# Optimization experiments

Measured on AMD Instinct MI355X. Metric: run time of the kernel, lower is better.

Reference implementation:

```python
import jax, jax.numpy as jnp
import numpy as np

N_FQK, N_FV, N_REL, N_VAL, N_KNOW = 512, 256, 128, 64, 256
TOPK_QK, TOPK_V, TOPK_REL, TOPK_VAL = 64, 32, 16, 3
FQK_END = N_FQK
FV_END = N_FQK + N_FV
REL_END = FV_END + N_REL
VAL_END = REL_END + N_VAL
TOTAL = VAL_END + N_KNOW


def setup_inputs() -> dict:
    key = jax.random.key(0)
    k1, k2, k3, k4, k5 = jax.random.split(key, 5)
    B, S, D, DS = 8, 4096, 1024, 64
    x = jax.random.normal(k1, (B, S, D), dtype=jnp.float32)
    importance = jax.random.uniform(k2, (B, S), dtype=jnp.float32)
    proj_w = jax.random.normal(k3, (DS, D), dtype=jnp.float32) * (1.0 / np.sqrt(D))
    proj_b = jax.random.normal(k4, (DS,), dtype=jnp.float32) * 0.01
    neuron_emb = jax.random.normal(k5, (TOTAL, DS), dtype=jnp.float32) * 0.02
    return {"x": x, "importance": importance, "proj_w": proj_w,
            "proj_b": proj_b, "neuron_emb": neuron_emb}


def _topk_sparsify(w, k):
    # keep top-k values per row, zero elsewhere
    vals, idx = jax.lax.top_k(w, k)
    B = w.shape[0]
    sparse = jnp.zeros_like(w).at[jnp.arange(B)[:, None], idx].set(vals)
    return sparse, idx


def reference(x, importance, proj_w, proj_b, neuron_emb):
    # shared projection + normalized neuron embeddings (eval: dropout off,
    # no excitability bonus)
    h = jnp.einsum('bsd,kd->bsk', x, proj_w) + proj_b          # [B,S,d_space]
    emb_n = neuron_emb / jnp.linalg.norm(neuron_emb, axis=-1, keepdims=True)
    all_logits = jnp.einsum('bsk,nk->bsn', h, emb_n)            # [B,S,TOTAL]

    def agg(logits):
        pref = jax.nn.softmax(logits, axis=-1)                  # [B,S,n]
        return jnp.einsum('bs,bsn->bn', importance, pref)

    w_qk = agg(all_logits[..., :FQK_END])
    _, idx_qk = jax.lax.top_k(w_qk, TOPK_QK)
    idx_qk = jnp.sort(idx_qk, axis=-1)

    w_v = agg(all_logits[..., FQK_END:FV_END])
    _, idx_v = jax.lax.top_k(w_v, TOPK_V)
    idx_v = jnp.sort(idx_v, axis=-1)

    rel_logits = all_logits[..., FV_END:REL_END]
    # relational_Q and relational_K use the same logits slice (eval mode)
    rel_dense_Q = agg(rel_logits)
    rel_dense_K = agg(rel_logits)
    rel_Q, _ = _topk_sparsify(rel_dense_Q, TOPK_REL)
    rel_K, _ = _topk_sparsify(rel_dense_K, TOPK_REL)

    val_dense = agg(all_logits[..., REL_END:VAL_END])
    val_w, _ = _topk_sparsify(val_dense, TOPK_VAL)

    return idx_qk, idx_v, rel_Q, rel_K, val_w
```

## Files before the change

kernel.cpp:

```cpp
#include <hip/hip_runtime.h>


typedef short short8 __attribute__((ext_vector_type(8)));
typedef float f32x4 __attribute__((ext_vector_type(4)));
typedef unsigned int uint4v __attribute__((ext_vector_type(4)));

__device__ __forceinline__ unsigned short f32_to_bf16(float f) {
  unsigned u = __float_as_uint(f);
  u += 0x7FFF + ((u >> 16) & 1);
  return (unsigned short)(u >> 16);
}
__device__ __forceinline__ float bf16_to_f32(unsigned short h) {
  return __uint_as_float(((unsigned)h) << 16);
}

__device__ __forceinline__ unsigned cvt_pk_bf16(float a, float b) {
  unsigned r;
  asm("v_cvt_pk_bf16_f32 %0, %1, %2" : "=v"(r) : "v"(a), "v"(b));
  return r;
}

__device__ __forceinline__ void split8v(const f32x4& v0, const f32x4& v1,
                                        short8& hi, short8& lo) {
  unsigned hp[4], lp[4];
#pragma unroll
  for (int j = 0; j < 4; ++j) {
    float a = (j < 2) ? v0[2 * j] : v1[2 * j - 4];
    float b = (j < 2) ? v0[2 * j + 1] : v1[2 * j - 3];
    unsigned p = cvt_pk_bf16(a, b);
    float ra = a - __uint_as_float(p << 16);
    float rb = b - __uint_as_float(p & 0xFFFF0000u);
    hp[j] = p;
    lp[j] = cvt_pk_bf16(ra, rb);
  }
  hi = __builtin_bit_cast(short8, (uint4v){hp[0], hp[1], hp[2], hp[3]});
  lo = __builtin_bit_cast(short8, (uint4v){lp[0], lp[1], lp[2], lp[3]});
}

#define MFMA(a, b, c) __builtin_amdgcn_mfma_f32_16x16x32_bf16(a, b, c, 0, 0, 0)
#define WAITVM(n) asm volatile("s_waitcnt vmcnt(" #n ")" ::: "memory")

typedef const __attribute__((address_space(1))) unsigned int guint;
typedef __attribute__((address_space(3))) unsigned int luint;
__device__ __forceinline__ void stage16(const float* g, float* l) {
  __builtin_amdgcn_global_load_lds((guint*)g, (luint*)l, 16, 0, 0);
}
__device__ __forceinline__ void bar() {
  asm volatile("" ::: "memory");
  __builtin_amdgcn_s_barrier();
  asm volatile("" ::: "memory");
}

__global__ __launch_bounds__(256) void k_prep(const float* __restrict__ pw,
                                              const float* __restrict__ emb,
                                              unsigned short* __restrict__ whi,
                                              unsigned short* __restrict__ wlo,
                                              unsigned short* __restrict__ ehi,
                                              unsigned short* __restrict__ elo) {
  int tid = blockIdx.x * 256 + threadIdx.x;
  for (int i = tid; i < 65536; i += gridDim.x * 256) {
    float v = pw[i];
    unsigned short h = f32_to_bf16(v);
    whi[i] = h;
    wlo[i] = f32_to_bf16(v - bf16_to_f32(h));
  }
  int wid = tid >> 6, lane = tid & 63;
  int nw = gridDim.x * 4;
  for (int n = wid; n < 960; n += nw) {
    float v = emb[n * 64 + lane];
    float s = v * v;
#pragma unroll
    for (int off = 1; off < 64; off <<= 1) s += __shfl_xor(s, off);
    float vn = v / sqrtf(s);
    unsigned short h = f32_to_bf16(vn);
    ehi[n * 64 + lane] = h;
    elo[n * 64 + lane] = f32_to_bf16(vn - bf16_to_f32(h));
  }
}

__global__ __launch_bounds__(256, 4) void k_main(
    const float* __restrict__ x, const unsigned short* __restrict__ whi,
    const unsigned short* __restrict__ wlo, const float* __restrict__ pb,
    const unsigned short* __restrict__ ehi, const unsigned short* __restrict__ elo,
    const float* __restrict__ imp, float* __restrict__ pp) {
  __shared__ __align__(16) float xt[5][32][32];
  __shared__ __align__(16) unsigned short hxh[32][64];
  __shared__ __align__(16) unsigned short hxl[32][64];
  __shared__ float zpart[4][32][4];
  __shared__ float coefL[32][4];

  const int tid = threadIdx.x, w = tid >> 6, lane = tid & 63;
  const int q = lane >> 4, c = lane & 15;
  const int row0 = blockIdx.x * 32;
  const int nt0 = w;
  const int koff = blockIdx.x & 31;

  const int srow = tid >> 3;
  const int scol = ((tid & 7) ^ (srow & 7)) * 4;
  const float* sbase = x + (size_t)(row0 + srow) * 1024 + scol;
  auto STAGEX = [&](int slot, int ks) {
    int kp = (ks + koff) & 31;
    stage16(sbase + kp * 32, &xt[slot][0][0] + (w << 8));
  };

  const unsigned short* bwh = whi + (size_t)(nt0 * 16 + c) * 1024 + q * 8;
  const unsigned short* bwl = wlo + (size_t)(nt0 * 16 + c) * 1024 + q * 8;

  f32x4 acc0 = {0.f, 0.f, 0.f, 0.f}, acc1 = {0.f, 0.f, 0.f, 0.f};

  const unsigned sw = (unsigned)((c & 7) << 4);
  const unsigned off1 = ((unsigned)(q * 32)) ^ sw;
  const unsigned off2 = ((unsigned)(q * 32 + 16)) ^ sw;
  const char* xby = (const char*)&xt[0][0][0] + (size_t)c * 128;

  int rs = 0, wsl = 4;
  auto projstep = [&](short8 B_hi, short8 B_lo) {
    const char* bp = xby + rs * 4096;
    f32x4 a0 = *(const f32x4*)(bp + off1);
    f32x4 a1 = *(const f32x4*)(bp + off2);
    f32x4 a2 = *(const f32x4*)(bp + 2048 + off1);
    f32x4 a3 = *(const f32x4*)(bp + 2048 + off2);
    short8 ah, al;
    split8v(a0, a1, ah, al);
    acc0 = MFMA(ah, B_hi, acc0);
    acc0 = MFMA(ah, B_lo, acc0);
    acc0 = MFMA(al, B_hi, acc0);
    split8v(a2, a3, ah, al);
    acc1 = MFMA(ah, B_hi, acc1);
    acc1 = MFMA(ah, B_lo, acc1);
    acc1 = MFMA(al, B_hi, acc1);
    ++rs; if (rs == 5) rs = 0;
  };
  auto loadB = [&](short8 (&h)[2], short8 (&l)[2], int g) {
    int k0 = (2 * g + koff) & 31, k1 = (2 * g + 1 + koff) & 31;
    h[0] = *(const short8*)(bwh + k0 * 32);
    h[1] = *(const short8*)(bwh + k1 * 32);
    l[0] = *(const short8*)(bwl + k0 * 32);
    l[1] = *(const short8*)(bwl + k1 * 32);
  };

  short8 BhA[2], BlA[2], BhB[2], BlB[2];
  loadB(BhA, BlA, 0);
  STAGEX(0, 0); STAGEX(1, 1); STAGEX(2, 2); STAGEX(3, 3);

  auto gpair = [&](int g) {
    loadB(BhB, BlB, g + 1);
    WAITVM(6); bar();
    STAGEX(wsl, 2 * g + 4); ++wsl; if (wsl == 5) wsl = 0;
    projstep(BhA[0], BlA[0]);
    WAITVM(7); bar();
    STAGEX(wsl, 2 * g + 5); ++wsl; if (wsl == 5) wsl = 0;
    projstep(BhA[1], BlA[1]);
    loadB(BhA, BlA, g + 2);
    WAITVM(6); bar();
    STAGEX(wsl, 2 * g + 6); ++wsl; if (wsl == 5) wsl = 0;
    projstep(BhB[0], BlB[0]);
    WAITVM(7); bar();
    STAGEX(wsl, 2 * g + 7); ++wsl; if (wsl == 5) wsl = 0;
    projstep(BhB[1], BlB[1]);
  };
  gpair(0); gpair(2); gpair(4); gpair(6); gpair(8); gpair(10); gpair(12);
  loadB(BhB, BlB, 15);
  WAITVM(7); bar(); projstep(BhA[0], BlA[0]);
  WAITVM(6); bar(); projstep(BhA[1], BlA[1]);
  WAITVM(1); bar(); projstep(BhB[0], BlB[0]);
  WAITVM(0); bar(); projstep(BhB[1], BlB[1]);

  float bias = pb[nt0 * 16 + c];
#pragma unroll
  for (int mt = 0; mt < 2; ++mt) {
    f32x4 a = mt ? acc1 : acc0;
#pragma unroll
    for (int r = 0; r < 4; ++r) {
      float val = a[r] + bias;
      int row = mt * 16 + q * 4 + r;
      unsigned colb = (unsigned)((nt0 * 16 + c) * 2);
      unsigned o = (unsigned)(row * 128) + (colb ^ ((unsigned)(row & 7) << 4));
      unsigned short h = f32_to_bf16(val);
      *(unsigned short*)((char*)&hxh[0][0] + o) = h;
      *(unsigned short*)((char*)&hxl[0][0] + o) = f32_to_bf16(val - bf16_to_f32(h));
    }
  }
  __syncthreads();

  short8 Ahi[2][2], Alo[2][2];
#pragma unroll
  for (int mt = 0; mt < 2; ++mt) {
    int row = mt * 16 + c;
    unsigned rsw = (unsigned)((row & 7) << 4);
#pragma unroll
    for (int k2 = 0; k2 < 2; ++k2) {
      unsigned o = (unsigned)(row * 128) + (((unsigned)(k2 * 64 + q * 16)) ^ rsw);
      Ahi[mt][k2] = *(const short8*)((const char*)&hxh[0][0] + o);
      Alo[mt][k2] = *(const short8*)((const char*)&hxl[0][0] + o);
    }
  }

  const size_t ebq = (size_t)c * 64 + q * 8;
  short8 eA[4], eB[4];
  auto LOADE = [&](short8 (&d)[4], int i) {
    size_t eb = (size_t)(w + 4 * i) * 1024 + ebq;
    d[0] = *(const short8*)(ehi + eb);
    d[1] = *(const short8*)(ehi + eb + 32);
    d[2] = *(const short8*)(elo + eb);
    d[3] = *(const short8*)(elo + eb + 32);
  };
  auto logits = [&](int mt, short8 (&e)[4]) -> f32x4 {
    f32x4 la = {0.f, 0.f, 0.f, 0.f}, lb = {0.f, 0.f, 0.f, 0.f};
    la = MFMA(Ahi[mt][0], e[0], la); la = MFMA(Ahi[mt][1], e[1], la);
    lb = MFMA(Ahi[mt][0], e[2], lb); lb = MFMA(Ahi[mt][1], e[3], lb);
    lb = MFMA(Alo[mt][0], e[0], lb); lb = MFMA(Alo[mt][1], e[1], lb);
    return la + lb;
  };

  f32x4 zacc0 = {0.f, 0.f, 0.f, 0.f}, zacc1 = {0.f, 0.f, 0.f, 0.f};
  auto zflush = [&](int seg) {
#pragma unroll
    for (int mt = 0; mt < 2; ++mt)
#pragma unroll
      for (int r = 0; r < 4; ++r) {
        float v = mt ? zacc1[r] : zacc0[r];
        v += __shfl_xor(v, 1); v += __shfl_xor(v, 2);
        v += __shfl_xor(v, 4); v += __shfl_xor(v, 8);
        if (c == 0) zpart[w][mt * 16 + q * 4 + r][seg] = v;
      }
    zacc0 = (f32x4){0.f, 0.f, 0.f, 0.f};
    zacc1 = (f32x4){0.f, 0.f, 0.f, 0.f};
  };

  int cur_seg = 0;
  auto step1 = [&](int i, short8 (&e)[4]) {
    int nt = w + 4 * i;
    int s = (nt < 32) ? 0 : (nt < 48) ? 1 : (nt < 56) ? 2 : 3;
    if (s != cur_seg) { zflush(cur_seg); cur_seg = s; }
    f32x4 l0 = logits(0, e), l1 = logits(1, e);
#pragma unroll
    for (int r = 0; r < 4; ++r) {
      zacc0[r] += __expf(l0[r]);
      zacc1[r] += __expf(l1[r]);
    }
  };
  LOADE(eA, 0);
#pragma unroll 1
  for (int j = 0; j < 7; ++j) {
    LOADE(eB, 2 * j + 1); step1(2 * j, eA);
    LOADE(eA, 2 * j + 2); step1(2 * j + 1, eB);
  }
  step1(14, eA);
  zflush(cur_seg);
  __syncthreads();
  if (tid < 128) {
    int row = tid & 31, sg = tid >> 5;
    float Z = zpart[0][row][sg] + zpart[1][row][sg] + zpart[2][row][sg] + zpart[3][row][sg];
    coefL[row][sg] = imp[row0 + row] / Z;
  }
  __syncthreads();

  float* ppb = pp + (size_t)blockIdx.x * 960;
  f32x4 cf0, cf1;
  int cs2 = -1;
  auto step2 = [&](int i, short8 (&e)[4]) {
    int nt = w + 4 * i;
    int s = (nt < 32) ? 0 : (nt < 48) ? 1 : (nt < 56) ? 2 : 3;
    if (s != cs2) {
#pragma unroll
      for (int r = 0; r < 4; ++r) {
        cf0[r] = coefL[q * 4 + r][s];
        cf1[r] = coefL[16 + q * 4 + r][s];
      }
      cs2 = s;
    }
    f32x4 l0 = logits(0, e), l1 = logits(1, e);
    float wsum = 0.f;
#pragma unroll
    for (int r = 0; r < 4; ++r) {
      wsum = fmaf(__expf(l0[r]), cf0[r], wsum);
      wsum = fmaf(__expf(l1[r]), cf1[r], wsum);
    }
    wsum += __shfl_xor(wsum, 16);
    wsum += __shfl_xor(wsum, 32);
    if (lane < 16) ppb[nt * 16 + c] = wsum;
  };
  LOADE(eA, 0);
#pragma unroll 1
  for (int j = 0; j < 7; ++j) {
    LOADE(eB, 2 * j + 1); step2(2 * j, eA);
    LOADE(eA, 2 * j + 2); step2(2 * j + 1, eB);
  }
  step2(14, eA);
}

__global__ __launch_bounds__(256) void k_topk(const float* __restrict__ pp,
                                              float* __restrict__ out) {
  __shared__ float vals[512];
  __shared__ int flags[512];
  int blk = blockIdx.x;
  int b = blk >> 2, t = blk & 3;
  int tid = threadIdx.x;
  const int Ns[4] = {512, 256, 128, 64};
  const int Ks[4] = {64, 32, 16, 3};
  const int Off[4] = {0, 512, 768, 896};
  int N = Ns[t], K = Ks[t], off = Off[t];
  for (int n = tid; n < N; n += 256) {
    const float* p = pp + (size_t)(b * 128) * 960 + off + n;
    float s0 = 0.f, s1 = 0.f, s2 = 0.f, s3 = 0.f;
    for (int rb = 0; rb < 128; rb += 4) {
      s0 += p[(size_t)(rb + 0) * 960];
      s1 += p[(size_t)(rb + 1) * 960];
      s2 += p[(size_t)(rb + 2) * 960];
      s3 += p[(size_t)(rb + 3) * 960];
    }
    vals[n] = (s0 + s1) + (s2 + s3);
  }
  __syncthreads();
  for (int n = tid; n < N; n += 256) {
    float v = vals[n];
    int rank = 0;
    for (int m = 0; m < N; ++m) {
      float u = vals[m];
      rank += (u > v || (u == v && m < n)) ? 1 : 0;
    }
    flags[n] = (rank < K) ? 1 : 0;
  }
  __syncthreads();
  if (t <= 1) {
    if (tid < 64) {
      int base = 0;
      for (int ch = 0; ch < N; ch += 64) {
        int n = ch + tid;
        int f = flags[n];
        unsigned long long mask = __ballot(f);
        if (f) {
          int pos = base + __popcll(mask & ((1ull << tid) - 1ull));
          if (t == 0) out[b * 64 + pos] = (float)n;
          else out[512 + b * 32 + pos] = (float)n;
        }
        base += __popcll(mask);
      }
    }
  } else if (t == 2) {
    for (int n = tid; n < 128; n += 256) {
      float v = flags[n] ? vals[n] : 0.f;
      out[768 + b * 128 + n] = v;
      out[1792 + b * 128 + n] = v;
    }
  } else {
    for (int n = tid; n < 64; n += 256) {
      float v = flags[n] ? vals[n] : 0.f;
      out[2816 + b * 64 + n] = v;
    }
  }
}

extern "C" void kernel_launch(void* const* d_in, const int* in_sizes, int n_in,
                              void* d_out, int out_size, void* d_ws, size_t ws_size,
                              hipStream_t stream) {
  const float* x   = (const float*)d_in[0];
  const float* imp = (const float*)d_in[1];
  const float* pw  = (const float*)d_in[2];
  const float* pb  = (const float*)d_in[3];
  const float* emb = (const float*)d_in[4];
  float* out = (float*)d_out;

  char* ws = (char*)d_ws;
  unsigned short* whi = (unsigned short*)(ws);
  unsigned short* wlo = (unsigned short*)(ws + 131072);
  unsigned short* ehi = (unsigned short*)(ws + 262144);
  unsigned short* elo = (unsigned short*)(ws + 385024);
  float*          pp  = (float*)(ws + 507904);

  hipLaunchKernelGGL(k_prep, dim3(64), dim3(256), 0, stream, pw, emb, whi, wlo, ehi, elo);
  hipLaunchKernelGGL(k_main, dim3(1024), dim3(256), 0, stream, x, whi, wlo, pb, ehi, elo, imp, pp);
  hipLaunchKernelGGL(k_topk, dim3(32), dim3(256), 0, stream, pp, out);
}
```

Before: 326.4 us.

## Halve row tile per block, interleave hi/lo weights, split partial reduction kernel

The main kernel now processes 16 rows per block instead of 32, so twice as many blocks run, with occupancy raised to 8 blocks per CU and a 3-slot, 64-wide x staging ring. Weights and embeddings are stored with hi/lo bf16 halves interleaved so each lane reads them from nearby addresses. The per-batch column reduction of partial sums moves into a separate, wider-parallel kernel ahead of top-k. The aim is more latency hiding and a cheaper tail, at the cost of fewer MFMAs per B-fragment load (half the reuse of weights per block), twice as many partial rows, and an extra kernel launch.

```diff
diff --git a/kernel.cpp b/kernel.cpp
--- a/kernel.cpp
+++ b/kernel.cpp
@@ -53,16 +53,17 @@
 
 __global__ __launch_bounds__(256) void k_prep(const float* __restrict__ pw,
                                               const float* __restrict__ emb,
-                                              unsigned short* __restrict__ whi,
-                                              unsigned short* __restrict__ wlo,
-                                              unsigned short* __restrict__ ehi,
-                                              unsigned short* __restrict__ elo) {
+                                              unsigned short* __restrict__ W2,
+                                              unsigned short* __restrict__ E2) {
   int tid = blockIdx.x * 256 + threadIdx.x;
   for (int i = tid; i < 65536; i += gridDim.x * 256) {
     float v = pw[i];
     unsigned short h = f32_to_bf16(v);
-    whi[i] = h;
-    wlo[i] = f32_to_bf16(v - bf16_to_f32(h));
+    int col = i >> 10, d = i & 1023;
+    int ks = d >> 5, q = (d >> 3) & 3, j = d & 7;
+    int idx = col * 2048 + ks * 64 + q * 16 + j;
+    W2[idx] = h;
+    W2[idx + 8] = f32_to_bf16(v - bf16_to_f32(h));
   }
   int wid = tid >> 6, lane = tid & 63;
   int nw = gridDim.x * 4;
@@ -73,159 +74,143 @@
     for (int off = 1; off < 64; off <<= 1) s += __shfl_xor(s, off);
     float vn = v / sqrtf(s);
     unsigned short h = f32_to_bf16(vn);
-    ehi[n * 64 + lane] = h;
-    elo[n * 64 + lane] = f32_to_bf16(vn - bf16_to_f32(h));
-  }
-}
-
-__global__ __launch_bounds__(256, 4) void k_main(
-    const float* __restrict__ x, const unsigned short* __restrict__ whi,
-    const unsigned short* __restrict__ wlo, const float* __restrict__ pb,
-    const unsigned short* __restrict__ ehi, const unsigned short* __restrict__ elo,
+    int idx = n * 128 + (lane >> 3) * 16 + (lane & 7);
+    E2[idx] = h;
+    E2[idx + 8] = f32_to_bf16(vn - bf16_to_f32(h));
+  }
+}
+
+__global__ __launch_bounds__(256, 8) void k_main(
+    const float* __restrict__ x, const unsigned short* __restrict__ W2,
+    const float* __restrict__ pb, const unsigned short* __restrict__ E2,
     const float* __restrict__ imp, float* __restrict__ pp) {
-  __shared__ __align__(16) float xt[5][32][32];
-  __shared__ __align__(16) unsigned short hxh[32][64];
-  __shared__ __align__(16) unsigned short hxl[32][64];
-  __shared__ float zpart[4][32][4];
-  __shared__ float coefL[32][4];
+  __shared__ __align__(16) float xt[3][16][64];
+  __shared__ __align__(16) unsigned short hxh[16][64];
+  __shared__ __align__(16) unsigned short hxl[16][64];
+  __shared__ float zpart[4][16][4];
+  __shared__ float coefL[16][4];
 
   const int tid = threadIdx.x, w = tid >> 6, lane = tid & 63;
   const int q = lane >> 4, c = lane & 15;
-  const int row0 = blockIdx.x * 32;
+  const int row0 = blockIdx.x * 16;
   const int nt0 = w;
-  const int koff = blockIdx.x & 31;
-
-  const int srow = tid >> 3;
-  const int scol = ((tid & 7) ^ (srow & 7)) * 4;
-  const float* sbase = x + (size_t)(row0 + srow) * 1024 + scol;
-  auto STAGEX = [&](int slot, int ks) {
-    int kp = (ks + koff) & 31;
-    stage16(sbase + kp * 32, &xt[slot][0][0] + (w << 8));
-  };
-
-  const unsigned short* bwh = whi + (size_t)(nt0 * 16 + c) * 1024 + q * 8;
-  const unsigned short* bwl = wlo + (size_t)(nt0 * 16 + c) * 1024 + q * 8;
-
-  f32x4 acc0 = {0.f, 0.f, 0.f, 0.f}, acc1 = {0.f, 0.f, 0.f, 0.f};
-
-  const unsigned sw = (unsigned)((c & 7) << 4);
-  const unsigned off1 = ((unsigned)(q * 32)) ^ sw;
-  const unsigned off2 = ((unsigned)(q * 32 + 16)) ^ sw;
-  const char* xby = (const char*)&xt[0][0][0] + (size_t)c * 128;
-
-  int rs = 0, wsl = 4;
-  auto projstep = [&](short8 B_hi, short8 B_lo) {
-    const char* bp = xby + rs * 4096;
-    f32x4 a0 = *(const f32x4*)(bp + off1);
-    f32x4 a1 = *(const f32x4*)(bp + off2);
-    f32x4 a2 = *(const f32x4*)(bp + 2048 + off1);
-    f32x4 a3 = *(const f32x4*)(bp + 2048 + off2);
+  const int uoff = blockIdx.x & 15;
+
+  const int srow = tid >> 4;
+  const int p16 = tid & 15;
+  const int lslot = (p16 & 8) | ((p16 & 7) ^ (srow & 7));
+  const float* sbase = x + (size_t)(row0 + srow) * 1024 + lslot * 4;
+  auto STAGEX = [&](int slot, int u) {
+    int up = (u + uoff) & 15;
+    stage16(sbase + up * 64, &xt[slot][0][0] + (w << 8));
+  };
+
+  const unsigned short* bw = W2 + (size_t)(nt0 * 16 + c) * 2048 + q * 16;
+
+  f32x4 acc = {0.f, 0.f, 0.f, 0.f};
+
+  const unsigned o0a = (unsigned)(c * 256 + (((q * 2) ^ (c & 7)) << 4));
+  const unsigned o0b = (unsigned)(c * 256 + (((q * 2 + 1) ^ (c & 7)) << 4));
+  const char* xbase = (const char*)&xt[0][0][0];
+
+  int rs = 0, wsl = 2;
+  auto projstep2 = [&](short8 (&bh)[2], short8 (&bl)[2]) {
+    const char* bp = xbase + rs * 4096;
+    f32x4 a0 = *(const f32x4*)(bp + o0a);
+    f32x4 a1 = *(const f32x4*)(bp + o0b);
     short8 ah, al;
     split8v(a0, a1, ah, al);
-    acc0 = MFMA(ah, B_hi, acc0);
-    acc0 = MFMA(ah, B_lo, acc0);
-    acc0 = MFMA(al, B_hi, acc0);
-    split8v(a2, a3, ah, al);
-    acc1 = MFMA(ah, B_hi, acc1);
-    acc1 = MFMA(ah, B_lo, acc1);
-    acc1 = MFMA(al, B_hi, acc1);
-    ++rs; if (rs == 5) rs = 0;
-  };
-  auto loadB = [&](short8 (&h)[2], short8 (&l)[2], int g) {
-    int k0 = (2 * g + koff) & 31, k1 = (2 * g + 1 + koff) & 31;
-    h[0] = *(const short8*)(bwh + k0 * 32);
-    h[1] = *(const short8*)(bwh + k1 * 32);
-    l[0] = *(const short8*)(bwl + k0 * 32);
-    l[1] = *(const short8*)(bwl + k1 * 32);
+    acc = MFMA(ah, bh[0], acc);
+    acc = MFMA(ah, bl[0], acc);
+    acc = MFMA(al, bh[0], acc);
+    a0 = *(const f32x4*)(bp + o0a + 128);
+    a1 = *(const f32x4*)(bp + o0b + 128);
+    split8v(a0, a1, ah, al);
+    acc = MFMA(ah, bh[1], acc);
+    acc = MFMA(ah, bl[1], acc);
+    acc = MFMA(al, bh[1], acc);
+    ++rs; if (rs == 3) rs = 0;
+  };
+  auto loadB = [&](short8 (&h)[2], short8 (&l)[2], int u) {
+    int ku = (u + uoff) & 15;
+    const unsigned short* f = bw + ku * 128;
+    h[0] = *(const short8*)(f);
+    l[0] = *(const short8*)(f + 8);
+    h[1] = *(const short8*)(f + 64);
+    l[1] = *(const short8*)(f + 72);
   };
 
   short8 BhA[2], BlA[2], BhB[2], BlB[2];
   loadB(BhA, BlA, 0);
-  STAGEX(0, 0); STAGEX(1, 1); STAGEX(2, 2); STAGEX(3, 3);
-
-  auto gpair = [&](int g) {
-    loadB(BhB, BlB, g + 1);
-    WAITVM(6); bar();
-    STAGEX(wsl, 2 * g + 4); ++wsl; if (wsl == 5) wsl = 0;
-    projstep(BhA[0], BlA[0]);
-    WAITVM(7); bar();
-    STAGEX(wsl, 2 * g + 5); ++wsl; if (wsl == 5) wsl = 0;
-    projstep(BhA[1], BlA[1]);
-    loadB(BhA, BlA, g + 2);
-    WAITVM(6); bar();
-    STAGEX(wsl, 2 * g + 6); ++wsl; if (wsl == 5) wsl = 0;
-    projstep(BhB[0], BlB[0]);
-    WAITVM(7); bar();
-    STAGEX(wsl, 2 * g + 7); ++wsl; if (wsl == 5) wsl = 0;
-    projstep(BhB[1], BlB[1]);
-  };
-  gpair(0); gpair(2); gpair(4); gpair(6); gpair(8); gpair(10); gpair(12);
+  STAGEX(0, 0); STAGEX(1, 1);
+  auto unit = [&](int u, short8 (&ch)[2], short8 (&cl)[2],
+                  short8 (&nh)[2], short8 (&nl)[2]) {
+    loadB(nh, nl, u + 1);
+    WAITVM(5); bar();
+    STAGEX(wsl, u + 2); ++wsl; if (wsl == 3) wsl = 0;
+    projstep2(ch, cl);
+  };
+  unit(0, BhA, BlA, BhB, BlB);  unit(1, BhB, BlB, BhA, BlA);
+  unit(2, BhA, BlA, BhB, BlB);  unit(3, BhB, BlB, BhA, BlA);
+  unit(4, BhA, BlA, BhB, BlB);  unit(5, BhB, BlB, BhA, BlA);
+  unit(6, BhA, BlA, BhB, BlB);  unit(7, BhB, BlB, BhA, BlA);
+  unit(8, BhA, BlA, BhB, BlB);  unit(9, BhB, BlB, BhA, BlA);
+  unit(10, BhA, BlA, BhB, BlB); unit(11, BhB, BlB, BhA, BlA);
+  unit(12, BhA, BlA, BhB, BlB); unit(13, BhB, BlB, BhA, BlA);
   loadB(BhB, BlB, 15);
-  WAITVM(7); bar(); projstep(BhA[0], BlA[0]);
-  WAITVM(6); bar(); projstep(BhA[1], BlA[1]);
-  WAITVM(1); bar(); projstep(BhB[0], BlB[0]);
-  WAITVM(0); bar(); projstep(BhB[1], BlB[1]);
+  WAITVM(5); bar(); projstep2(BhA, BlA);
+  WAITVM(0); bar(); projstep2(BhB, BlB);
 
   float bias = pb[nt0 * 16 + c];
 #pragma unroll
-  for (int mt = 0; mt < 2; ++mt) {
-    f32x4 a = mt ? acc1 : acc0;
-#pragma unroll
-    for (int r = 0; r < 4; ++r) {
-      float val = a[r] + bias;
-      int row = mt * 16 + q * 4 + r;
-      unsigned colb = (unsigned)((nt0 * 16 + c) * 2);
-      unsigned o = (unsigned)(row * 128) + (colb ^ ((unsigned)(row & 7) << 4));
-      unsigned short h = f32_to_bf16(val);
-      *(unsigned short*)((char*)&hxh[0][0] + o) = h;
-      *(unsigned short*)((char*)&hxl[0][0] + o) = f32_to_bf16(val - bf16_to_f32(h));
-    }
-  }
-  __syncthreads();
-
-  short8 Ahi[2][2], Alo[2][2];
-#pragma unroll
-  for (int mt = 0; mt < 2; ++mt) {
-    int row = mt * 16 + c;
-    unsigned rsw = (unsigned)((row & 7) << 4);
+  for (int r = 0; r < 4; ++r) {
+    float val = acc[r] + bias;
+    int row = q * 4 + r;
+    unsigned colb = (unsigned)((nt0 * 16 + c) * 2);
+    unsigned o = (unsigned)(row * 128) + (colb ^ ((unsigned)(row & 7) << 4));
+    unsigned short h = f32_to_bf16(val);
+    *(unsigned short*)((char*)&hxh[0][0] + o) = h;
+    *(unsigned short*)((char*)&hxl[0][0] + o) = f32_to_bf16(val - bf16_to_f32(h));
+  }
+  __syncthreads();
+
+  short8 Ahi[2], Alo[2];
+  {
+    unsigned rsw = (unsigned)((c & 7) << 4);
 #pragma unroll
     for (int k2 = 0; k2 < 2; ++k2) {
-      unsigned o = (unsigned)(row * 128) + (((unsigned)(k2 * 64 + q * 16)) ^ rsw);
-      Ahi[mt][k2] = *(const short8*)((const char*)&hxh[0][0] + o);
-      Alo[mt][k2] = *(const short8*)((const char*)&hxl[0][0] + o);
-    }
-  }
-
-  const size_t ebq = (size_t)c * 64 + q * 8;
+      unsigned o = (unsigned)(c * 128) + (((unsigned)(k2 * 64 + q * 16)) ^ rsw);
+      Ahi[k2] = *(const short8*)((const char*)&hxh[0][0] + o);
+      Alo[k2] = *(const short8*)((const char*)&hxl[0][0] + o);
+    }
+  }
+
   short8 eA[4], eB[4];
   auto LOADE = [&](short8 (&d)[4], int i) {
-    size_t eb = (size_t)(w + 4 * i) * 1024 + ebq;
-    d[0] = *(const short8*)(ehi + eb);
-    d[1] = *(const short8*)(ehi + eb + 32);
-    d[2] = *(const short8*)(elo + eb);
-    d[3] = *(const short8*)(elo + eb + 32);
-  };
-  auto logits = [&](int mt, short8 (&e)[4]) -> f32x4 {
+    const unsigned short* e = E2 + (size_t)((w + 4 * i) * 16 + c) * 128 + q * 16;
+    d[0] = *(const short8*)(e);
+    d[1] = *(const short8*)(e + 64);
+    d[2] = *(const short8*)(e + 8);
+    d[3] = *(const short8*)(e + 72);
+  };
+  auto logits = [&](short8 (&e)[4]) -> f32x4 {
     f32x4 la = {0.f, 0.f, 0.f, 0.f}, lb = {0.f, 0.f, 0.f, 0.f};
-    la = MFMA(Ahi[mt][0], e[0], la); la = MFMA(Ahi[mt][1], e[1], la);
-    lb = MFMA(Ahi[mt][0], e[2], lb); lb = MFMA(Ahi[mt][1], e[3], lb);
-    lb = MFMA(Alo[mt][0], e[0], lb); lb = MFMA(Alo[mt][1], e[1], lb);
+    la = MFMA(Ahi[0], e[0], la); la = MFMA(Ahi[1], e[1], la);
+    lb = MFMA(Ahi[0], e[2], lb); lb = MFMA(Ahi[1], e[3], lb);
+    lb = MFMA(Alo[0], e[0], lb); lb = MFMA(Alo[1], e[1], lb);
     return la + lb;
   };
 
-  f32x4 zacc0 = {0.f, 0.f, 0.f, 0.f}, zacc1 = {0.f, 0.f, 0.f, 0.f};
+  f32x4 zacc = {0.f, 0.f, 0.f, 0.f};
   auto zflush = [&](int seg) {
 #pragma unroll
-    for (int mt = 0; mt < 2; ++mt)
-#pragma unroll
-      for (int r = 0; r < 4; ++r) {
-        float v = mt ? zacc1[r] : zacc0[r];
-        v += __shfl_xor(v, 1); v += __shfl_xor(v, 2);
-        v += __shfl_xor(v, 4); v += __shfl_xor(v, 8);
-        if (c == 0) zpart[w][mt * 16 + q * 4 + r][seg] = v;
-      }
-    zacc0 = (f32x4){0.f, 0.f, 0.f, 0.f};
-    zacc1 = (f32x4){0.f, 0.f, 0.f, 0.f};
+    for (int r = 0; r < 4; ++r) {
+      float v = zacc[r];
+      v += __shfl_xor(v, 1); v += __shfl_xor(v, 2);
+      v += __shfl_xor(v, 4); v += __shfl_xor(v, 8);
+      if (c == 0) zpart[w][q * 4 + r][seg] = v;
+    }
+    zacc = (f32x4){0.f, 0.f, 0.f, 0.f};
   };
 
   int cur_seg = 0;
@@ -233,12 +218,9 @@
     int nt = w + 4 * i;
     int s = (nt < 32) ? 0 : (nt < 48) ? 1 : (nt < 56) ? 2 : 3;
     if (s != cur_seg) { zflush(cur_seg); cur_seg = s; }
-    f32x4 l0 = logits(0, e), l1 = logits(1, e);
-#pragma unroll
-    for (int r = 0; r < 4; ++r) {
-      zacc0[r] += __expf(l0[r]);
-      zacc1[r] += __expf(l1[r]);
-    }
+    f32x4 l = logits(e);
+#pragma unroll
+    for (int r = 0; r < 4; ++r) zacc[r] += __expf(l[r]);
   };
   LOADE(eA, 0);
 #pragma unroll 1
@@ -249,34 +231,28 @@
   step1(14, eA);
   zflush(cur_seg);
   __syncthreads();
-  if (tid < 128) {
-    int row = tid & 31, sg = tid >> 5;
+  if (tid < 64) {
+    int row = tid & 15, sg = tid >> 4;
     float Z = zpart[0][row][sg] + zpart[1][row][sg] + zpart[2][row][sg] + zpart[3][row][sg];
     coefL[row][sg] = imp[row0 + row] / Z;
   }
   __syncthreads();
 
   float* ppb = pp + (size_t)blockIdx.x * 960;
-  f32x4 cf0, cf1;
+  f32x4 cf;
   int cs2 = -1;
   auto step2 = [&](int i, short8 (&e)[4]) {
     int nt = w + 4 * i;
     int s = (nt < 32) ? 0 : (nt < 48) ? 1 : (nt < 56) ? 2 : 3;
     if (s != cs2) {
 #pragma unroll
-      for (int r = 0; r < 4; ++r) {
-        cf0[r] = coefL[q * 4 + r][s];
-        cf1[r] = coefL[16 + q * 4 + r][s];
-      }
+      for (int r = 0; r < 4; ++r) cf[r] = coefL[q * 4 + r][s];
       cs2 = s;
     }
-    f32x4 l0 = logits(0, e), l1 = logits(1, e);
+    f32x4 l = logits(e);
     float wsum = 0.f;
 #pragma unroll
-    for (int r = 0; r < 4; ++r) {
-      wsum = fmaf(__expf(l0[r]), cf0[r], wsum);
-      wsum = fmaf(__expf(l1[r]), cf1[r], wsum);
-    }
+    for (int r = 0; r < 4; ++r) wsum = fmaf(__expf(l[r]), cf[r], wsum);
     wsum += __shfl_xor(wsum, 16);
     wsum += __shfl_xor(wsum, 32);
     if (lane < 16) ppb[nt * 16 + c] = wsum;
@@ -290,7 +266,25 @@
   step2(14, eA);
 }
 
-__global__ __launch_bounds__(256) void k_topk(const float* __restrict__ pp,
+__global__ __launch_bounds__(256) void k_red(const float* __restrict__ pp,
+                                             float* __restrict__ wg2) {
+  __shared__ float red[4][64];
+  int bx = blockIdx.x, b = bx / 15, ch = bx % 15;
+  int t = threadIdx.x, col = t & 63, rq = t >> 6;
+  const float* p = pp + (size_t)(b * 256 + rq * 64) * 960 + ch * 64 + col;
+  float s0 = 0.f, s1 = 0.f, s2 = 0.f, s3 = 0.f;
+  for (int k = 0; k < 64; k += 4) {
+    s0 += p[(size_t)(k + 0) * 960];
+    s1 += p[(size_t)(k + 1) * 960];
+    s2 += p[(size_t)(k + 2) * 960];
+    s3 += p[(size_t)(k + 3) * 960];
+  }
+  red[rq][col] = (s0 + s1) + (s2 + s3);
+  __syncthreads();
+  if (t < 64) wg2[b * 960 + ch * 64 + t] = red[0][t] + red[1][t] + red[2][t] + red[3][t];
+}
+
+__global__ __launch_bounds__(256) void k_topk(const float* __restrict__ wg2,
                                               float* __restrict__ out) {
   __shared__ float vals[512];
   __shared__ int flags[512];
@@ -301,17 +295,7 @@
   const int Ks[4] = {64, 32, 16, 3};
   const int Off[4] = {0, 512, 768, 896};
   int N = Ns[t], K = Ks[t], off = Off[t];
-  for (int n = tid; n < N; n += 256) {
-    const float* p = pp + (size_t)(b * 128) * 960 + off + n;
-    float s0 = 0.f, s1 = 0.f, s2 = 0.f, s3 = 0.f;
-    for (int rb = 0; rb < 128; rb += 4) {
-      s0 += p[(size_t)(rb + 0) * 960];
-      s1 += p[(size_t)(rb + 1) * 960];
-      s2 += p[(size_t)(rb + 2) * 960];
-      s3 += p[(size_t)(rb + 3) * 960];
-    }
-    vals[n] = (s0 + s1) + (s2 + s3);
-  }
+  for (int n = tid; n < N; n += 256) vals[n] = wg2[b * 960 + off + n];
   __syncthreads();
   for (int n = tid; n < N; n += 256) {
     float v = vals[n];
@@ -363,13 +347,13 @@
   float* out = (float*)d_out;
 
   char* ws = (char*)d_ws;
-  unsigned short* whi = (unsigned short*)(ws);
-  unsigned short* wlo = (unsigned short*)(ws + 131072);
-  unsigned short* ehi = (unsigned short*)(ws + 262144);
-  unsigned short* elo = (unsigned short*)(ws + 385024);
-  float*          pp  = (float*)(ws + 507904);
-
-  hipLaunchKernelGGL(k_prep, dim3(64), dim3(256), 0, stream, pw, emb, whi, wlo, ehi, elo);
-  hipLaunchKernelGGL(k_main, dim3(1024), dim3(256), 0, stream, x, whi, wlo, pb, ehi, elo, imp, pp);
-  hipLaunchKernelGGL(k_topk, dim3(32), dim3(256), 0, stream, pp, out);
-}
+  unsigned short* W2 = (unsigned short*)(ws);
+  unsigned short* E2 = (unsigned short*)(ws + 262144);
+  float*          pp = (float*)(ws + 507904);
+  float*         wg2 = (float*)(ws + 8372224);
+
+  hipLaunchKernelGGL(k_prep, dim3(64), dim3(256), 0, stream, pw, emb, W2, E2);
+  hipLaunchKernelGGL(k_main, dim3(2048), dim3(256), 0, stream, x, W2, pb, E2, imp, pp);
+  hipLaunchKernelGGL(k_red,  dim3(120), dim3(256), 0, stream, pp, wg2);
+  hipLaunchKernelGGL(k_topk, dim3(32), dim3(256), 0, stream, wg2, out);
+}
```

After: 429.5 us. +31.6%, slower.
